# Optimization experiments

Hardware: AMD Instinct MI355X
Metric: run time of the kernel (lower is better)

Reference implementation:

```python
import jax, jax.numpy as jnp
import numpy as np

D_MODEL = 1024
D_STATE = 128
D_CONV = 4
EXPAND = 2
HEADDIM = 64
D_INNER = EXPAND * D_MODEL          # 2048
NHEADS = D_INNER // HEADDIM         # 32
NGROUPS = 1
CONV_DIM = D_INNER + 2 * NGROUPS * D_STATE            # 2304
D_IN_PROJ = 2 * D_INNER + 2 * NGROUPS * D_STATE + NHEADS  # 4384
NUM_CLASS = 48
BATCH = 2
SEQLEN = 512


def setup_inputs() -> dict:
    key = jax.random.key(0)
    ks = jax.random.split(key, 8)
    s = 0.02
    inputs = jax.random.normal(ks[0], (BATCH, SEQLEN, D_MODEL), jnp.float32)
    W_in = jax.random.normal(ks[1], (D_MODEL, D_IN_PROJ), jnp.float32) * s
    conv_w = jax.random.normal(ks[2], (CONV_DIM, D_CONV), jnp.float32) * 0.2
    conv_b = jnp.zeros((CONV_DIM,), jnp.float32)
    # dt_bias = inverse-softplus of dt sampled in [1e-3, 0.1] (mamba init)
    dt = jnp.exp(jax.random.uniform(ks[3], (NHEADS,), jnp.float32) * (np.log(0.1) - np.log(1e-3)) + np.log(1e-3))
    dt_bias = dt + jnp.log(-jnp.expm1(-dt))
    A_log = jnp.log(jax.random.uniform(ks[4], (NHEADS,), jnp.float32, 1.0, 16.0))
    D = jnp.ones((NHEADS,), jnp.float32)
    norm_w = jnp.ones((D_INNER,), jnp.float32)
    W_out = jax.random.normal(ks[5], (D_INNER, D_MODEL), jnp.float32) * s
    W_cls = jax.random.normal(ks[6], (D_INNER, NUM_CLASS), jnp.float32) * s
    b_cls = jnp.zeros((NUM_CLASS,), jnp.float32)
    return {"inputs": inputs, "W_in": W_in, "conv_w": conv_w, "conv_b": conv_b,
            "dt_bias": dt_bias, "A_log": A_log, "D": D, "norm_w": norm_w,
            "W_out": W_out, "W_cls": W_cls, "b_cls": b_cls}


def _forward(inputs, W_in, conv_w, conv_b, dt_bias, A_log, D, norm_w, W_out, W_cls, b_cls):
    B, L, _ = inputs.shape
    zxbcdt = inputs @ W_in                                     # (B,L,4384)
    z, xBC, dt = jnp.split(zxbcdt, [D_INNER, D_INNER + CONV_DIM], axis=-1)
    dt = jax.nn.softplus(dt + dt_bias)                         # (B,L,H)
    # causal depthwise conv over time on (x,B,C)
    xBC_t = jnp.pad(jnp.transpose(xBC, (0, 2, 1)), ((0, 0), (0, 0), (D_CONV - 1, 0)))
    xBC_c = jax.lax.conv_general_dilated(xBC_t, conv_w[:, None, :], (1,), 'VALID',
                                         feature_group_count=CONV_DIM)
    xBC = jax.nn.silu(jnp.transpose(xBC_c, (0, 2, 1)) + conv_b)
    x, Bm, Cm = jnp.split(xBC, [D_INNER, D_INNER + D_STATE], axis=-1)
    x = x.reshape(B, L, NHEADS, HEADDIM)
    A = -jnp.exp(A_log)                                        # (H,)
    dA = jnp.exp(dt * A)                                       # (B,L,H)

    def step(state, inp):
        # state: (B,H,P,N) -- selective SSM recurrence (chunk_size=1 path)
        x_t, B_t, C_t, dt_t, dA_t = inp
        state = state * dA_t[:, :, None, None] + jnp.einsum('bhp,bn,bh->bhpn', x_t, B_t, dt_t)
        y_t = jnp.einsum('bhpn,bn->bhp', state, C_t)
        return state, y_t

    state0 = jnp.zeros((B, NHEADS, HEADDIM, D_STATE), inputs.dtype)
    xs = (jnp.transpose(x, (1, 0, 2, 3)), jnp.transpose(Bm, (1, 0, 2)),
          jnp.transpose(Cm, (1, 0, 2)), jnp.transpose(dt, (1, 0, 2)),
          jnp.transpose(dA, (1, 0, 2)))
    _, ys = jax.lax.scan(step, state0, xs)                     # ys: (L,B,H,P)
    y = jnp.transpose(ys, (1, 0, 2, 3)) + D[None, None, :, None] * x
    y = y.reshape(B, L, D_INNER)
    # gated RMSNorm: rmsnorm(y * silu(z)) * weight
    y = y * jax.nn.silu(z)
    y = y * jax.lax.rsqrt(jnp.mean(y * y, axis=-1, keepdims=True) + 1e-5) * norm_w
    # hidden_states (d_inner=2048) go through the per-timestep classifier
    preds = y @ W_cls + b_cls                                  # (B,L,num_class)
    return preds


def reference(inputs, W_in, conv_w, conv_b, dt_bias, A_log, D, norm_w, W_out, W_cls, b_cls):
    return _forward(inputs, W_in, conv_w, conv_b, dt_bias, A_log, D, norm_w, W_out, W_cls, b_cls)
```

## Files before the change

kernel.cpp:

```cpp
#include <hip/hip_runtime.h>
#include <hip/hip_bf16.h>
#include <cstdint>

#define BATCH 2
#define SEQLEN 512
#define BL (BATCH*SEQLEN)
#define DMODEL 1024
#define DINNER 2048
#define NHEADS 32
#define HEADDIM 64
#define DSTATE 128
#define CONVDIM 2304
#define DINPROJ 4384
#define NPROJPAD 4480
#define NCLS 48
#define QC 64
#define NCH 8

typedef short bf16x8 __attribute__((ext_vector_type(8)));
typedef float f32x4  __attribute__((ext_vector_type(4)));
typedef unsigned int u32;
typedef const __attribute__((address_space(1))) u32 gu32;
typedef __attribute__((address_space(3))) u32 lu32;

static __device__ __forceinline__ void gl16(const void* g, void* l) {
    __builtin_amdgcn_global_load_lds((gu32*)g, (lu32*)l, 16, 0, 0);
}

static __device__ __forceinline__ unsigned short f2bf(float f) {
    unsigned u = __float_as_uint(f);
    unsigned r = (u + 0x7FFFu + ((u >> 16) & 1u)) >> 16;
    return (unsigned short)r;
}

__global__ __launch_bounds__(256) void k_cvt_a(const float* __restrict__ in,
                                               unsigned short* __restrict__ out) {
    int i = (blockIdx.x * 256 + threadIdx.x) * 4;
    float4 v = *(const float4*)(in + i);
    ushort4 o;
    o.x = f2bf(v.x); o.y = f2bf(v.y); o.z = f2bf(v.z); o.w = f2bf(v.w);
    *(ushort4*)(out + i) = o;
}

__global__ __launch_bounds__(256) void k_transpose_w(const float* __restrict__ W,
                                                     unsigned short* __restrict__ Wt) {
    __shared__ float tile[32][33];
    int n0 = blockIdx.x * 32;
    int k0 = blockIdx.y * 32;
    int tx = threadIdx.x & 31;
    int ty = threadIdx.x >> 5;
#pragma unroll
    for (int i = 0; i < 4; ++i) {
        int k = k0 + ty + i * 8;
        tile[ty + i * 8][tx] = W[(size_t)k * DINPROJ + n0 + tx];
    }
    __syncthreads();
#pragma unroll
    for (int i = 0; i < 4; ++i) {
        int n = n0 + ty + i * 8;
        Wt[(size_t)n * DMODEL + k0 + tx] = f2bf(tile[tx][ty + i * 8]);
    }
}

__global__ __launch_bounds__(256) void k_prep_cls(const float* __restrict__ W,
                                                  const float* __restrict__ bcls,
                                                  unsigned short* __restrict__ Wt,
                                                  float* __restrict__ out) {
    int bid = blockIdx.x;
    if (bid < 192) {
        int i = bid * 256 + threadIdx.x;
        out[i] = bcls[i % NCLS];
    } else {
        int n = bid - 192;
        for (int k = threadIdx.x; k < DINNER; k += 256)
            Wt[(size_t)n * DINNER + k] = f2bf(W[(size_t)k * NCLS + n]);
    }
}

__global__ __launch_bounds__(256) void k_gemm_in(const unsigned short* __restrict__ A,
                                                 const unsigned short* __restrict__ Bt,
                                                 float* __restrict__ C) {
    __shared__ unsigned short As[128 * 32];
    __shared__ unsigned short Bs[128 * 32];
    const int tid  = threadIdx.x;
    const int m0   = blockIdx.y * 128;
    const int n0   = blockIdx.x * 128;
    const int w    = tid >> 6;
    const int lane = tid & 63;
    const int wm   = w >> 1, wn = w & 1;
    const int fr   = lane & 15, fq = lane >> 4;
    const int srow = w * 16 + (lane >> 2);
    const int skg  = (lane & 3) * 8;
    const unsigned short* gA0 = A  + (size_t)(m0 + srow) * DMODEL + skg;
    const unsigned short* gA1 = gA0 + (size_t)64 * DMODEL;
    const unsigned short* gB0 = Bt + (size_t)(n0 + srow) * DMODEL + skg;
    const unsigned short* gB1 = gB0 + (size_t)64 * DMODEL;
    unsigned short* lA0 = As + w * 512;
    unsigned short* lA1 = As + 2048 + w * 512;
    unsigned short* lB0 = Bs + w * 512;
    unsigned short* lB1 = Bs + 2048 + w * 512;

    f32x4 acc[4][4] = {};
    for (int k0 = 0; k0 < DMODEL; k0 += 32) {
        __syncthreads();
        gl16(gA0 + k0, lA0);
        gl16(gA1 + k0, lA1);
        gl16(gB0 + k0, lB0);
        gl16(gB1 + k0, lB1);
        __syncthreads();
        bf16x8 af[4], bf[4];
#pragma unroll
        for (int mt = 0; mt < 4; ++mt)
            af[mt] = *(const bf16x8*)(&As[(wm * 64 + mt * 16 + fr) * 32 + fq * 8]);
#pragma unroll
        for (int nt = 0; nt < 4; ++nt)
            bf[nt] = *(const bf16x8*)(&Bs[(wn * 64 + nt * 16 + fr) * 32 + fq * 8]);
#pragma unroll
        for (int mt = 0; mt < 4; ++mt)
#pragma unroll
            for (int nt = 0; nt < 4; ++nt)
                acc[mt][nt] = __builtin_amdgcn_mfma_f32_16x16x32_bf16(af[mt], bf[nt], acc[mt][nt], 0, 0, 0);
    }
#pragma unroll
    for (int mt = 0; mt < 4; ++mt) {
#pragma unroll
        for (int nt = 0; nt < 4; ++nt) {
            int col = n0 + wn * 64 + nt * 16 + fr;
            if (col < DINPROJ) {
#pragma unroll
                for (int r = 0; r < 4; ++r) {
                    int row = m0 + wm * 64 + mt * 16 + fq * 4 + r;
                    C[(size_t)row * DINPROJ + col] = acc[mt][nt][r];
                }
            }
        }
    }
}

__global__ __launch_bounds__(256) void k_conv_dt(const float* __restrict__ zx,
                                                 const float* __restrict__ conv_w,
                                                 const float* __restrict__ conv_b,
                                                 const float* __restrict__ dt_bias,
                                                 float* __restrict__ xbc,
                                                 float* __restrict__ dtb) {
    int row = blockIdx.y;
    int c   = blockIdx.x * 256 + threadIdx.x;
    int b = row >> 9, l = row & 511;
    if (c < CONVDIM) {
        float acc = conv_b[c];
#pragma unroll
        for (int j = 0; j < 4; ++j) {
            int ls = l - 3 + j;
            float v = (ls >= 0) ? zx[((size_t)(b * SEQLEN + ls)) * DINPROJ + DINNER + c] : 0.f;
            acc += v * conv_w[c * 4 + j];
        }
        float s = acc / (1.f + expf(-acc));
        xbc[(size_t)row * CONVDIM + c] = s;
    } else if (c < CONVDIM + NHEADS) {
        int h = c - CONVDIM;
        float raw = zx[(size_t)row * DINPROJ + (DINNER + CONVDIM) + h] + dt_bias[h];
        float dt = (raw > 20.f) ? raw : log1pf(expf(raw));
        dtb[row * NHEADS + h] = dt;
    }
}

__global__ __launch_bounds__(256) void k_chunk(const float* __restrict__ xbc,
                                               const float* __restrict__ dtb,
                                               const float* __restrict__ A_log,
                                               const float* __restrict__ Dvec,
                                               float* __restrict__ yb,
                                               float* __restrict__ Sc_g,
                                               float* __restrict__ lam_g,
                                               float* __restrict__ esc_g) {
    const int gid = blockIdx.x;
    const int c = gid & 7;
    const int h = (gid >> 3) & 31;
    const int b = gid >> 8;
    const int row0 = b * SEQLEN + c * QC;

    __shared__ float cumS[QC], wS[QC], dtS[QC];
    __shared__ unsigned short Xt[QC][72];
    __shared__ unsigned short Bs[QC][136];
    __shared__ unsigned short BtW[DSTATE][72];
    __shared__ unsigned short Cs[QC][136];
    __shared__ unsigned short Gs[QC][72];

    const int tid = threadIdx.x;
    if (tid < 64) {
        float dtv = dtb[(size_t)(row0 + tid) * NHEADS + h];
        float nA = -expf(A_log[h]);
        float x = dtv * nA;
#pragma unroll
        for (int off = 1; off < 64; off <<= 1) {
            float v = __shfl_up(x, off, 64);
            if (tid >= off) x += v;
        }
        float cumTot = __shfl(x, 63, 64);
        cumS[tid] = x;
        dtS[tid] = dtv;
        wS[tid] = expf(cumTot - x) * dtv;
        esc_g[(size_t)gid * QC + tid] = expf(x);
        if (tid == 0) lam_g[gid] = expf(cumTot);
    }
    __syncthreads();

    {
        int row = tid >> 2;
        int g = tid & 3;
        const float* rp = xbc + (size_t)(row0 + row) * CONVDIM;
        float wrow = wS[row];
#pragma unroll
        for (int i = 0; i < 4; ++i) {
            float4 v = *(const float4*)(rp + h * HEADDIM + g * 16 + i * 4);
            int p = g * 16 + i * 4;
            Xt[p + 0][row] = f2bf(v.x);
            Xt[p + 1][row] = f2bf(v.y);
            Xt[p + 2][row] = f2bf(v.z);
            Xt[p + 3][row] = f2bf(v.w);
        }
#pragma unroll
        for (int i = 0; i < 8; ++i) {
            int n = g * 32 + i * 4;
            float4 v = *(const float4*)(rp + DINNER + n);
            ushort4 u;
            u.x = f2bf(v.x); u.y = f2bf(v.y); u.z = f2bf(v.z); u.w = f2bf(v.w);
            *(ushort4*)(&Bs[row][n]) = u;
            BtW[n + 0][row] = f2bf(v.x * wrow);
            BtW[n + 1][row] = f2bf(v.y * wrow);
            BtW[n + 2][row] = f2bf(v.z * wrow);
            BtW[n + 3][row] = f2bf(v.w * wrow);
        }
#pragma unroll
        for (int i = 0; i < 8; ++i) {
            int n = g * 32 + i * 4;
            float4 v = *(const float4*)(rp + DINNER + DSTATE + n);
            ushort4 u;
            u.x = f2bf(v.x); u.y = f2bf(v.y); u.z = f2bf(v.z); u.w = f2bf(v.w);
            *(ushort4*)(&Cs[row][n]) = u;
        }
    }
    __syncthreads();

    const int w = tid >> 6, lane = tid & 63;
    const int fr = lane & 15, fq = lane >> 4, fk = (lane >> 4) * 8;

    f32x4 accG[4] = {};
#pragma unroll
    for (int kk = 0; kk < 4; ++kk) {
        bf16x8 a = *(const bf16x8*)(&Cs[w * 16 + fr][kk * 32 + fk]);
#pragma unroll
        for (int nt = 0; nt < 4; ++nt) {
            bf16x8 bb = *(const bf16x8*)(&Bs[nt * 16 + fr][kk * 32 + fk]);
            accG[nt] = __builtin_amdgcn_mfma_f32_16x16x32_bf16(a, bb, accG[nt], 0, 0, 0);
        }
    }
#pragma unroll
    for (int nt = 0; nt < 4; ++nt) {
        int s = nt * 16 + fr;
        float cs = cumS[s], dts = dtS[s];
#pragma unroll
        for (int r = 0; r < 4; ++r) {
            int t = w * 16 + fq * 4 + r;
            float val = (s <= t) ? accG[nt][r] * expf(cumS[t] - cs) * dts : 0.f;
            Gs[t][s] = f2bf(val);
        }
    }
    __syncthreads();

    f32x4 accY[4] = {};
#pragma unroll
    for (int kk = 0; kk < 2; ++kk) {
        bf16x8 a = *(const bf16x8*)(&Gs[w * 16 + fr][kk * 32 + fk]);
#pragma unroll
        for (int pt = 0; pt < 4; ++pt) {
            bf16x8 bb = *(const bf16x8*)(&Xt[pt * 16 + fr][kk * 32 + fk]);
            accY[pt] = __builtin_amdgcn_mfma_f32_16x16x32_bf16(a, bb, accY[pt], 0, 0, 0);
        }
    }
    f32x4 accS[8] = {};
#pragma unroll
    for (int kk = 0; kk < 2; ++kk) {
        bf16x8 a = *(const bf16x8*)(&Xt[w * 16 + fr][kk * 32 + fk]);
#pragma unroll
        for (int nt = 0; nt < 8; ++nt) {
            bf16x8 bb = *(const bf16x8*)(&BtW[nt * 16 + fr][kk * 32 + fk]);
            accS[nt] = __builtin_amdgcn_mfma_f32_16x16x32_bf16(a, bb, accS[nt], 0, 0, 0);
        }
    }
    float Dh = Dvec[h];
#pragma unroll
    for (int pt = 0; pt < 4; ++pt) {
        int p = pt * 16 + fr;
#pragma unroll
        for (int r = 0; r < 4; ++r) {
            int t = w * 16 + fq * 4 + r;
            float xv = xbc[(size_t)(row0 + t) * CONVDIM + h * HEADDIM + p];
            yb[(size_t)(row0 + t) * DINNER + h * HEADDIM + p] = accY[pt][r] + Dh * xv;
        }
    }
    float* scp = Sc_g + (size_t)gid * (HEADDIM * DSTATE);
#pragma unroll
    for (int nt = 0; nt < 8; ++nt) {
        int n = nt * 16 + fr;
#pragma unroll
        for (int r = 0; r < 4; ++r) {
            int p = w * 16 + fq * 4 + r;
            scp[p * DSTATE + n] = accS[nt][r];
        }
    }
}

__global__ __launch_bounds__(256) void k_chain(const float* __restrict__ Sc_g,
                                               const float* __restrict__ lam_g,
                                               unsigned short* __restrict__ Sin_bf) {
    int bh = blockIdx.x;
    int tid = threadIdx.x;
    float s[32];
#pragma unroll
    for (int i = 0; i < 32; ++i) s[i] = 0.f;
    for (int c = 0; c < NCH; ++c) {
        size_t base = (size_t)(bh * NCH + c) * (HEADDIM * DSTATE) + tid * 32;
#pragma unroll
        for (int j = 0; j < 32; j += 4) {
            ushort4 u;
            u.x = f2bf(s[j + 0]); u.y = f2bf(s[j + 1]);
            u.z = f2bf(s[j + 2]); u.w = f2bf(s[j + 3]);
            *(ushort4*)(Sin_bf + base + j) = u;
        }
        float lam = lam_g[bh * NCH + c];
#pragma unroll
        for (int j = 0; j < 32; j += 4) {
            float4 v = *(const float4*)(Sc_g + base + j);
            s[j + 0] = s[j + 0] * lam + v.x;
            s[j + 1] = s[j + 1] * lam + v.y;
            s[j + 2] = s[j + 2] * lam + v.z;
            s[j + 3] = s[j + 3] * lam + v.w;
        }
    }
}

__global__ __launch_bounds__(256) void k_cross(const float* __restrict__ xbc,
                                               const float* __restrict__ esc_g,
                                               const unsigned short* __restrict__ Sin_bf,
                                               float* __restrict__ yb) {
    const int gid = blockIdx.x;
    const int c = gid & 7;
    const int h = (gid >> 3) & 31;
    const int b = gid >> 8;
    const int row0 = b * SEQLEN + c * QC;
    __shared__ unsigned short Ct[QC][136];
    __shared__ unsigned short Ss[QC][136];
    const int tid = threadIdx.x;
    {
        int row = tid >> 2, g = tid & 3;
        const float* rp = xbc + (size_t)(row0 + row) * CONVDIM + DINNER + DSTATE;
        float esc = esc_g[(size_t)gid * QC + row];
#pragma unroll
        for (int i = 0; i < 8; ++i) {
            int n = g * 32 + i * 4;
            float4 v = *(const float4*)(rp + n);
            ushort4 u;
            u.x = f2bf(v.x * esc); u.y = f2bf(v.y * esc);
            u.z = f2bf(v.z * esc); u.w = f2bf(v.w * esc);
            *(ushort4*)(&Ct[row][n]) = u;
        }
        const uint4* sp = (const uint4*)(Sin_bf + (size_t)gid * (HEADDIM * DSTATE));
#pragma unroll
        for (int i = 0; i < 4; ++i) {
            uint4 v = sp[row * 16 + g * 4 + i];
            *(uint4*)(&Ss[row][g * 32 + i * 8]) = v;
        }
    }
    __syncthreads();
    const int w = tid >> 6, lane = tid & 63;
    const int fr = lane & 15, fq = lane >> 4, fk = (lane >> 4) * 8;
    f32x4 acc[4] = {};
#pragma unroll
    for (int kk = 0; kk < 4; ++kk) {
        bf16x8 a = *(const bf16x8*)(&Ct[w * 16 + fr][kk * 32 + fk]);
#pragma unroll
        for (int pt = 0; pt < 4; ++pt) {
            bf16x8 bb = *(const bf16x8*)(&Ss[pt * 16 + fr][kk * 32 + fk]);
            acc[pt] = __builtin_amdgcn_mfma_f32_16x16x32_bf16(a, bb, acc[pt], 0, 0, 0);
        }
    }
#pragma unroll
    for (int pt = 0; pt < 4; ++pt) {
        int p = pt * 16 + fr;
#pragma unroll
        for (int r = 0; r < 4; ++r) {
            int t = w * 16 + fq * 4 + r;
            size_t yi = (size_t)(row0 + t) * DINNER + h * HEADDIM + p;
            yb[yi] += acc[pt][r];
        }
    }
}

__global__ __launch_bounds__(256) void k_gate_norm(const float* __restrict__ zx,
                                                   const float* __restrict__ nw,
                                                   const float* __restrict__ y,
                                                   unsigned short* __restrict__ Gbf) {
    int row = blockIdx.x;
    int tid = threadIdx.x;
    const float* zrow = zx + (size_t)row * DINPROJ;
    const float* yr = y + (size_t)row * DINNER;
    float g[8];
    float ss = 0.f;
#pragma unroll
    for (int i = 0; i < 2; ++i) {
        int c = tid * 4 + i * 1024;
        float4 yv = *(const float4*)(yr + c);
        float4 zv = *(const float4*)(zrow + c);
        float zs[4] = {zv.x, zv.y, zv.z, zv.w};
        float ys[4] = {yv.x, yv.y, yv.z, yv.w};
#pragma unroll
        for (int k = 0; k < 4; ++k) {
            float sil = zs[k] / (1.f + expf(-zs[k]));
            float gg = ys[k] * sil;
            g[i * 4 + k] = gg;
            ss += gg * gg;
        }
    }
#pragma unroll
    for (int off = 32; off >= 1; off >>= 1) ss += __shfl_xor(ss, off, 64);
    __shared__ float wsum[4];
    if ((tid & 63) == 0) wsum[tid >> 6] = ss;
    __syncthreads();
    float tot = wsum[0] + wsum[1] + wsum[2] + wsum[3];
    float scale = rsqrtf(tot / (float)DINNER + 1e-5f);
#pragma unroll
    for (int i = 0; i < 2; ++i) {
        int c = tid * 4 + i * 1024;
        float4 nv = *(const float4*)(nw + c);
        ushort4 o;
        o.x = f2bf(g[i * 4 + 0] * scale * nv.x);
        o.y = f2bf(g[i * 4 + 1] * scale * nv.y);
        o.z = f2bf(g[i * 4 + 2] * scale * nv.z);
        o.w = f2bf(g[i * 4 + 3] * scale * nv.w);
        *(ushort4*)(Gbf + (size_t)row * DINNER + c) = o;
    }
}

__global__ __launch_bounds__(256) void k_cls_mfma(const unsigned short* __restrict__ G,
                                                  const unsigned short* __restrict__ Wt,
                                                  float* __restrict__ out) {
    __shared__ unsigned short Gs[64][72];
    __shared__ unsigned short Ws[48][72];
    const int m0  = blockIdx.x * 64;
    const int k00 = blockIdx.y * 256;
    const int tid = threadIdx.x;
    const int w = tid >> 6, lane = tid & 63;
    const int fr = lane & 15, fq = lane >> 4, fk = fq * 8;
    f32x4 acc[3] = {};
    for (int ks = 0; ks < 4; ++ks) {
        int k0 = k00 + ks * 64;
        __syncthreads();
        {
            int row = tid >> 2, seg = (tid & 3) * 16;
            const unsigned short* gp = G + (size_t)(m0 + row) * DINNER + k0 + seg;
            *(uint4*)(&Gs[row][seg])     = *(const uint4*)(gp);
            *(uint4*)(&Gs[row][seg + 8]) = *(const uint4*)(gp + 8);
        }
        if (tid < 192) {
            int row = tid >> 2, seg = (tid & 3) * 16;
            const unsigned short* wp = Wt + (size_t)row * DINNER + k0 + seg;
            *(uint4*)(&Ws[row][seg])     = *(const uint4*)(wp);
            *(uint4*)(&Ws[row][seg + 8]) = *(const uint4*)(wp + 8);
        }
        __syncthreads();
#pragma unroll
        for (int kk = 0; kk < 2; ++kk) {
            bf16x8 a = *(const bf16x8*)(&Gs[w * 16 + fr][kk * 32 + fk]);
#pragma unroll
            for (int nt = 0; nt < 3; ++nt) {
                bf16x8 bb = *(const bf16x8*)(&Ws[nt * 16 + fr][kk * 32 + fk]);
                acc[nt] = __builtin_amdgcn_mfma_f32_16x16x32_bf16(a, bb, acc[nt], 0, 0, 0);
            }
        }
    }
#pragma unroll
    for (int nt = 0; nt < 3; ++nt) {
        int col = nt * 16 + fr;
#pragma unroll
        for (int r = 0; r < 4; ++r) {
            int row = m0 + w * 16 + fq * 4 + r;
            atomicAdd(&out[(size_t)row * NCLS + col], acc[nt][r]);
        }
    }
}

extern "C" void kernel_launch(void* const* d_in, const int* in_sizes, int n_in,
                              void* d_out, int out_size, void* d_ws, size_t ws_size,
                              hipStream_t stream) {
    const float* inputs  = (const float*)d_in[0];
    const float* W_in    = (const float*)d_in[1];
    const float* conv_w  = (const float*)d_in[2];
    const float* conv_b  = (const float*)d_in[3];
    const float* dt_bias = (const float*)d_in[4];
    const float* A_log   = (const float*)d_in[5];
    const float* Dvec    = (const float*)d_in[6];
    const float* norm_w  = (const float*)d_in[7];
    const float* W_cls   = (const float*)d_in[9];
    const float* b_cls   = (const float*)d_in[10];
    float* out = (float*)d_out;

    float* ws   = (float*)d_ws;
    float* zx   = ws;
    float* xbc  = zx   + (size_t)BL * DINPROJ;
    float* dtb  = xbc  + (size_t)BL * CONVDIM;
    float* yb   = dtb  + (size_t)BL * NHEADS;
    float* Sc_g = yb   + (size_t)BL * DINNER;
    float* lam_g= Sc_g + (size_t)BATCH * NHEADS * NCH * HEADDIM * DSTATE;
    float* esc_g= lam_g+ (size_t)BATCH * NHEADS * NCH;
    unsigned short* Sin_bf = (unsigned short*)(esc_g + (size_t)BATCH * NHEADS * NCH * QC);
    unsigned short* abf    = Sin_bf + (size_t)BATCH * NHEADS * NCH * HEADDIM * DSTATE;
    unsigned short* wtbf   = abf + (size_t)BL * DMODEL;
    unsigned short* wclsbf = wtbf + (size_t)NPROJPAD * DMODEL;
    unsigned short* Gbf    = (unsigned short*)Sc_g;

    k_cvt_a<<<dim3(BL * DMODEL / (256 * 4)), dim3(256), 0, stream>>>(inputs, abf);
    k_transpose_w<<<dim3(DINPROJ / 32, DMODEL / 32), dim3(256), 0, stream>>>(W_in, wtbf);
    k_prep_cls<<<dim3(240), dim3(256), 0, stream>>>(W_cls, b_cls, wclsbf, out);
    k_gemm_in<<<dim3(NPROJPAD / 128, BL / 128), dim3(256), 0, stream>>>(abf, wtbf, zx);
    k_conv_dt<<<dim3(10, BL), dim3(256), 0, stream>>>(zx, conv_w, conv_b, dt_bias, xbc, dtb);
    k_chunk<<<dim3(BATCH * NHEADS * NCH), dim3(256), 0, stream>>>(xbc, dtb, A_log, Dvec,
                                                                  yb, Sc_g, lam_g, esc_g);
    k_chain<<<dim3(BATCH * NHEADS), dim3(256), 0, stream>>>(Sc_g, lam_g, Sin_bf);
    k_cross<<<dim3(BATCH * NHEADS * NCH), dim3(256), 0, stream>>>(xbc, esc_g, Sin_bf, yb);
    k_gate_norm<<<dim3(BL), dim3(256), 0, stream>>>(zx, norm_w, yb, Gbf);
    k_cls_mfma<<<dim3(BL / 64, 8), dim3(256), 0, stream>>>(Gbf, wclsbf, out);
}
```

Before: 184.1 us.

## Store in-proj output as bf16, deepen GEMM K step, split chain kernel

The input-projection GEMM now writes its output in bf16 instead of fp32, halving the store traffic and the later reads in the conv and gate-norm kernels, which convert back with a shift. The GEMM also stages 64 K-elements per barrier pair instead of 32, halving the synchronisation count. The inter-chunk state chain kernel is split four ways across the state dimension to launch more blocks. Rounding z, x, B, C and dt to bf16 adds precision loss.

```diff
diff --git a/kernel.cpp b/kernel.cpp
--- a/kernel.cpp
+++ b/kernel.cpp
@@ -32,6 +32,9 @@
     unsigned r = (u + 0x7FFFu + ((u >> 16) & 1u)) >> 16;
     return (unsigned short)r;
 }
+static __device__ __forceinline__ float bf2f(unsigned short u) {
+    return __uint_as_float(((unsigned)u) << 16);
+}
 
 __global__ __launch_bounds__(256) void k_cvt_a(const float* __restrict__ in,
                                                unsigned short* __restrict__ out) {
@@ -79,9 +82,9 @@
 
 __global__ __launch_bounds__(256) void k_gemm_in(const unsigned short* __restrict__ A,
                                                  const unsigned short* __restrict__ Bt,
-                                                 float* __restrict__ C) {
-    __shared__ unsigned short As[128 * 32];
-    __shared__ unsigned short Bs[128 * 32];
+                                                 unsigned short* __restrict__ C) {
+    __shared__ unsigned short As[2 * 4096];
+    __shared__ unsigned short Bs[2 * 4096];
     const int tid  = threadIdx.x;
     const int m0   = blockIdx.y * 128;
     const int n0   = blockIdx.x * 128;
@@ -95,31 +98,34 @@
     const unsigned short* gA1 = gA0 + (size_t)64 * DMODEL;
     const unsigned short* gB0 = Bt + (size_t)(n0 + srow) * DMODEL + skg;
     const unsigned short* gB1 = gB0 + (size_t)64 * DMODEL;
-    unsigned short* lA0 = As + w * 512;
-    unsigned short* lA1 = As + 2048 + w * 512;
-    unsigned short* lB0 = Bs + w * 512;
-    unsigned short* lB1 = Bs + 2048 + w * 512;
 
     f32x4 acc[4][4] = {};
-    for (int k0 = 0; k0 < DMODEL; k0 += 32) {
+    for (int k0 = 0; k0 < DMODEL; k0 += 64) {
         __syncthreads();
-        gl16(gA0 + k0, lA0);
-        gl16(gA1 + k0, lA1);
-        gl16(gB0 + k0, lB0);
-        gl16(gB1 + k0, lB1);
+#pragma unroll
+        for (int hh = 0; hh < 2; ++hh) {
+            int kg = k0 + hh * 32;
+            gl16(gA0 + kg, As + hh * 4096 + w * 512);
+            gl16(gA1 + kg, As + hh * 4096 + 2048 + w * 512);
+            gl16(gB0 + kg, Bs + hh * 4096 + w * 512);
+            gl16(gB1 + kg, Bs + hh * 4096 + 2048 + w * 512);
+        }
         __syncthreads();
-        bf16x8 af[4], bf[4];
-#pragma unroll
-        for (int mt = 0; mt < 4; ++mt)
-            af[mt] = *(const bf16x8*)(&As[(wm * 64 + mt * 16 + fr) * 32 + fq * 8]);
-#pragma unroll
-        for (int nt = 0; nt < 4; ++nt)
-            bf[nt] = *(const bf16x8*)(&Bs[(wn * 64 + nt * 16 + fr) * 32 + fq * 8]);
-#pragma unroll
-        for (int mt = 0; mt < 4; ++mt)
+#pragma unroll
+        for (int hh = 0; hh < 2; ++hh) {
+            bf16x8 af[4], bf[4];
+#pragma unroll
+            for (int mt = 0; mt < 4; ++mt)
+                af[mt] = *(const bf16x8*)(&As[hh * 4096 + (wm * 64 + mt * 16 + fr) * 32 + fq * 8]);
 #pragma unroll
             for (int nt = 0; nt < 4; ++nt)
-                acc[mt][nt] = __builtin_amdgcn_mfma_f32_16x16x32_bf16(af[mt], bf[nt], acc[mt][nt], 0, 0, 0);
+                bf[nt] = *(const bf16x8*)(&Bs[hh * 4096 + (wn * 64 + nt * 16 + fr) * 32 + fq * 8]);
+#pragma unroll
+            for (int mt = 0; mt < 4; ++mt)
+#pragma unroll
+                for (int nt = 0; nt < 4; ++nt)
+                    acc[mt][nt] = __builtin_amdgcn_mfma_f32_16x16x32_bf16(af[mt], bf[nt], acc[mt][nt], 0, 0, 0);
+        }
     }
 #pragma unroll
     for (int mt = 0; mt < 4; ++mt) {
@@ -130,14 +136,14 @@
 #pragma unroll
                 for (int r = 0; r < 4; ++r) {
                     int row = m0 + wm * 64 + mt * 16 + fq * 4 + r;
-                    C[(size_t)row * DINPROJ + col] = acc[mt][nt][r];
+                    C[(size_t)row * DINPROJ + col] = f2bf(acc[mt][nt][r]);
                 }
             }
         }
     }
 }
 
-__global__ __launch_bounds__(256) void k_conv_dt(const float* __restrict__ zx,
+__global__ __launch_bounds__(256) void k_conv_dt(const unsigned short* __restrict__ zx,
                                                  const float* __restrict__ conv_w,
                                                  const float* __restrict__ conv_b,
                                                  const float* __restrict__ dt_bias,
@@ -151,14 +157,14 @@
 #pragma unroll
         for (int j = 0; j < 4; ++j) {
             int ls = l - 3 + j;
-            float v = (ls >= 0) ? zx[((size_t)(b * SEQLEN + ls)) * DINPROJ + DINNER + c] : 0.f;
+            float v = (ls >= 0) ? bf2f(zx[((size_t)(b * SEQLEN + ls)) * DINPROJ + DINNER + c]) : 0.f;
             acc += v * conv_w[c * 4 + j];
         }
         float s = acc / (1.f + expf(-acc));
         xbc[(size_t)row * CONVDIM + c] = s;
     } else if (c < CONVDIM + NHEADS) {
         int h = c - CONVDIM;
-        float raw = zx[(size_t)row * DINPROJ + (DINNER + CONVDIM) + h] + dt_bias[h];
+        float raw = bf2f(zx[(size_t)row * DINPROJ + (DINNER + CONVDIM) + h]) + dt_bias[h];
         float dt = (raw > 20.f) ? raw : log1pf(expf(raw));
         dtb[row * NHEADS + h] = dt;
     }
@@ -313,15 +319,16 @@
 __global__ __launch_bounds__(256) void k_chain(const float* __restrict__ Sc_g,
                                                const float* __restrict__ lam_g,
                                                unsigned short* __restrict__ Sin_bf) {
-    int bh = blockIdx.x;
+    int bh = blockIdx.x >> 2;
+    int sl = blockIdx.x & 3;
     int tid = threadIdx.x;
-    float s[32];
-#pragma unroll
-    for (int i = 0; i < 32; ++i) s[i] = 0.f;
+    float s[8];
+#pragma unroll
+    for (int i = 0; i < 8; ++i) s[i] = 0.f;
     for (int c = 0; c < NCH; ++c) {
-        size_t base = (size_t)(bh * NCH + c) * (HEADDIM * DSTATE) + tid * 32;
-#pragma unroll
-        for (int j = 0; j < 32; j += 4) {
+        size_t base = (size_t)(bh * NCH + c) * (HEADDIM * DSTATE) + sl * 2048 + tid * 8;
+#pragma unroll
+        for (int j = 0; j < 8; j += 4) {
             ushort4 u;
             u.x = f2bf(s[j + 0]); u.y = f2bf(s[j + 1]);
             u.z = f2bf(s[j + 2]); u.w = f2bf(s[j + 3]);
@@ -329,7 +336,7 @@
         }
         float lam = lam_g[bh * NCH + c];
 #pragma unroll
-        for (int j = 0; j < 32; j += 4) {
+        for (int j = 0; j < 8; j += 4) {
             float4 v = *(const float4*)(Sc_g + base + j);
             s[j + 0] = s[j + 0] * lam + v.x;
             s[j + 1] = s[j + 1] * lam + v.y;
@@ -396,13 +403,13 @@
     }
 }
 
-__global__ __launch_bounds__(256) void k_gate_norm(const float* __restrict__ zx,
+__global__ __launch_bounds__(256) void k_gate_norm(const unsigned short* __restrict__ zx,
                                                    const float* __restrict__ nw,
                                                    const float* __restrict__ y,
                                                    unsigned short* __restrict__ Gbf) {
     int row = blockIdx.x;
     int tid = threadIdx.x;
-    const float* zrow = zx + (size_t)row * DINPROJ;
+    const unsigned short* zrow = zx + (size_t)row * DINPROJ;
     const float* yr = y + (size_t)row * DINNER;
     float g[8];
     float ss = 0.f;
@@ -410,8 +417,8 @@
     for (int i = 0; i < 2; ++i) {
         int c = tid * 4 + i * 1024;
         float4 yv = *(const float4*)(yr + c);
-        float4 zv = *(const float4*)(zrow + c);
-        float zs[4] = {zv.x, zv.y, zv.z, zv.w};
+        ushort4 zv = *(const ushort4*)(zrow + c);
+        float zs[4] = {bf2f(zv.x), bf2f(zv.y), bf2f(zv.z), bf2f(zv.w)};
         float ys[4] = {yv.x, yv.y, yv.z, yv.w};
 #pragma unroll
         for (int k = 0; k < 4; ++k) {
@@ -505,8 +512,8 @@
     float* out = (float*)d_out;
 
     float* ws   = (float*)d_ws;
-    float* zx   = ws;
-    float* xbc  = zx   + (size_t)BL * DINPROJ;
+    unsigned short* zxb = (unsigned short*)ws;
+    float* xbc  = ws   + (size_t)BL * DINPROJ / 2 + 512;
     float* dtb  = xbc  + (size_t)BL * CONVDIM;
     float* yb   = dtb  + (size_t)BL * NHEADS;
     float* Sc_g = yb   + (size_t)BL * DINNER;
@@ -521,12 +528,12 @@
     k_cvt_a<<<dim3(BL * DMODEL / (256 * 4)), dim3(256), 0, stream>>>(inputs, abf);
     k_transpose_w<<<dim3(DINPROJ / 32, DMODEL / 32), dim3(256), 0, stream>>>(W_in, wtbf);
     k_prep_cls<<<dim3(240), dim3(256), 0, stream>>>(W_cls, b_cls, wclsbf, out);
-    k_gemm_in<<<dim3(NPROJPAD / 128, BL / 128), dim3(256), 0, stream>>>(abf, wtbf, zx);
-    k_conv_dt<<<dim3(10, BL), dim3(256), 0, stream>>>(zx, conv_w, conv_b, dt_bias, xbc, dtb);
+    k_gemm_in<<<dim3(NPROJPAD / 128, BL / 128), dim3(256), 0, stream>>>(abf, wtbf, zxb);
+    k_conv_dt<<<dim3(10, BL), dim3(256), 0, stream>>>(zxb, conv_w, conv_b, dt_bias, xbc, dtb);
     k_chunk<<<dim3(BATCH * NHEADS * NCH), dim3(256), 0, stream>>>(xbc, dtb, A_log, Dvec,
                                                                   yb, Sc_g, lam_g, esc_g);
-    k_chain<<<dim3(BATCH * NHEADS), dim3(256), 0, stream>>>(Sc_g, lam_g, Sin_bf);
+    k_chain<<<dim3(BATCH * NHEADS * 4), dim3(256), 0, stream>>>(Sc_g, lam_g, Sin_bf);
     k_cross<<<dim3(BATCH * NHEADS * NCH), dim3(256), 0, stream>>>(xbc, esc_g, Sin_bf, yb);
-    k_gate_norm<<<dim3(BL), dim3(256), 0, stream>>>(zx, norm_w, yb, Gbf);
+    k_gate_norm<<<dim3(BL), dim3(256), 0, stream>>>(zxb, norm_w, yb, Gbf);
     k_cls_mfma<<<dim3(BL / 64, 8), dim3(256), 0, stream>>>(Gbf, wclsbf, out);
 }
```

Result: faster. 171.4 us (-6.9%).
